# Kernel optimization log

Measured on AMD Instinct MI355X. Metric: run time of the kernel, lower is better.

Reference implementation:

```python
import jax, jax.numpy as jnp
import numpy as np

B, S, D = 4, 1024, 1024
H = 16
HD = D // H  # head_dim = 64


def setup_inputs() -> dict:
    key = jax.random.key(0)
    k1, k2, k3 = jax.random.split(key, 3)
    x = jax.random.normal(k1, (B, S, D), dtype=jnp.float32)
    # qkv_proj: Linear(input_dim, 3*embed_dim), stored as (in, out) for x @ W
    scale = 1.0 / np.sqrt(D)
    W_qkv = jax.random.uniform(k2, (D, 3 * D), dtype=jnp.float32, minval=-scale, maxval=scale)
    b_qkv = jax.random.uniform(k3, (3 * D,), dtype=jnp.float32, minval=-scale, maxval=scale)
    return {"x": x, "W_qkv": W_qkv, "b_qkv": b_qkv}


def reference(x, W_qkv, b_qkv):
    b, s, _ = x.shape
    qkv = x @ W_qkv + b_qkv                       # [B,S,3D]
    qkv = qkv.reshape(b, s, H, 3 * HD)            # [B,S,H,3*hd]
    qkv = qkv.transpose(0, 2, 1, 3)               # [B,H,S,3*hd]
    q, k, v = jnp.split(qkv, 3, axis=-1)          # each [B,H,S,hd]
    scores = jnp.einsum('bhqd,bhkd->bhqk', q, k) / jnp.sqrt(jnp.float32(HD))
    attn = jax.nn.softmax(scores, axis=-1)        # [B,H,S,S]
    out = jnp.einsum('bhqk,bhkd->bhqd', attn, v)  # [B,H,S,hd]
    values = out.transpose(0, 2, 1, 3).reshape(b, s, H * HD)  # [B,S,D]
    return values
```

## Files before the change

kernel.cpp:

```cpp
#include <hip/hip_runtime.h>
#include <hip/hip_bf16.h>
#include <stdint.h>

#define BATCH 4
#define SEQ 1024
#define DMODEL 1024
#define NH 16
#define HD 64

typedef __attribute__((ext_vector_type(8))) short short8;
typedef __attribute__((ext_vector_type(4))) float f32x4;
typedef __attribute__((ext_vector_type(4))) unsigned short ushort4v;

__device__ __forceinline__ unsigned short f2bf(float f) {
    union { float f; uint32_t u; } v; v.f = f;
    uint32_t r = v.u + 0x7fff + ((v.u >> 16) & 1);
    return (unsigned short)(r >> 16);
}

__device__ __forceinline__ uint32_t pack2bf(float lo, float hi) {
    union { __hip_bfloat162 h; uint32_t u; } cv;
    cv.h = __float22bfloat162_rn(make_float2(lo, hi));
    return cv.u;
}

__global__ __launch_bounds__(256) void prep_kernel(const float* __restrict__ x,
                                                   const float* __restrict__ W,
                                                   unsigned short* __restrict__ xb,
                                                   unsigned short* __restrict__ Wt) {
    __shared__ float tile[32][33];
    int bid = blockIdx.x;
    if (bid < 2048) {
        int t = bid * 256 + threadIdx.x;
        const float4* p = (const float4*)x + (size_t)t * 2;
        float4 a = p[0], b = p[1];
        short8 o;
        o[0] = (short)f2bf(a.x); o[1] = (short)f2bf(a.y);
        o[2] = (short)f2bf(a.z); o[3] = (short)f2bf(a.w);
        o[4] = (short)f2bf(b.x); o[5] = (short)f2bf(b.y);
        o[6] = (short)f2bf(b.z); o[7] = (short)f2bf(b.w);
        *((short8*)xb + t) = o;
    } else {
        int r = bid - 2048;
        int nb = (r % 96) * 32;
        int kb = (r / 96) * 32;
        int tx = threadIdx.x & 31;
        int ty = threadIdx.x >> 5;
#pragma unroll
        for (int i = 0; i < 4; i++) {
            int k = kb + ty + i * 8;
            tile[ty + i * 8][tx] = W[(size_t)k * 3072 + nb + tx];
        }
        __syncthreads();
#pragma unroll
        for (int i = 0; i < 4; i++) {
            int n = nb + ty + i * 8;
            Wt[(size_t)n * 1024 + kb + tx] = f2bf(tile[tx][ty + i * 8]);
        }
    }
}

#define BM 128
#define BN 128
#define BKK 64
#define QSCALE 0.18033688011112042f

__global__ __launch_bounds__(256, 3) void qkv_gemm_kernel(
    const unsigned short* __restrict__ xb,
    const unsigned short* __restrict__ wt,
    const float* __restrict__ bias,
    unsigned short* __restrict__ Qb,
    unsigned short* __restrict__ Kb,
    unsigned short* __restrict__ VbT)
{
    __shared__ __align__(16) unsigned short As[BM][64];
    __shared__ __align__(16) unsigned short Bs[BN][64];
    int tid = threadIdx.x;
    int wave = tid >> 6, lane = tid & 63;
    int quad = lane >> 4, l16 = lane & 15;
    int wm = wave >> 1, wn = wave & 1;

    int id = blockIdx.x;
    int x = id & 7, r = id >> 3;
    int m_t = (x & 3) * 8 + (r & 7);
    int n_t = (x >> 2) * 12 + (r >> 3);
    int m0 = m_t * BM;
    int n0 = n_t * BN;

    int grow = lane >> 3;
    int gcol = ((lane & 7) ^ grow) << 3;
    const unsigned short* gA = xb + (size_t)(m0 + wave * 32 + grow) * 1024 + gcol;
    const unsigned short* gB = wt + (size_t)(n0 + wave * 32 + grow) * 1024 + gcol;
    unsigned short* ldsA = &As[wave * 32][0] + lane * 8;
    unsigned short* ldsB = &Bs[wave * 32][0] + lane * 8;
    int sw = l16 & 7;

    short8 areg[4], breg[4];
#pragma unroll
    for (int i = 0; i < 4; i++) {
        areg[i] = *(const short8*)(gA + (size_t)i * 8 * 1024);
        breg[i] = *(const short8*)(gB + (size_t)i * 8 * 1024);
    }

    f32x4 acc[4][4] = {};
    for (int k0 = 0; k0 < 1024; k0 += BKK) {
        __syncthreads();
#pragma unroll
        for (int i = 0; i < 4; i++) {
            *(short8*)(ldsA + i * 512) = areg[i];
            *(short8*)(ldsB + i * 512) = breg[i];
        }
        __syncthreads();
        if (k0 + BKK < 1024) {
#pragma unroll
            for (int i = 0; i < 4; i++) {
                areg[i] = *(const short8*)(gA + (size_t)i * 8 * 1024 + k0 + BKK);
                breg[i] = *(const short8*)(gB + (size_t)i * 8 * 1024 + k0 + BKK);
            }
        }
#pragma unroll
        for (int kk = 0; kk < BKK; kk += 32) {
            int kb = kk >> 3;
            short8 af[4], bf[4];
#pragma unroll
            for (int t = 0; t < 4; t++) {
                int ar = wm * 64 + t * 16 + l16;
                af[t] = *(const short8*)&As[ar][((kb + quad) ^ sw) << 3];
            }
#pragma unroll
            for (int t = 0; t < 4; t++) {
                int br = wn * 64 + t * 16 + l16;
                bf[t] = *(const short8*)&Bs[br][((kb + quad) ^ sw) << 3];
            }
#pragma unroll
            for (int mt = 0; mt < 4; mt++)
#pragma unroll
                for (int nt = 0; nt < 4; nt++)
                    acc[mt][nt] = __builtin_amdgcn_mfma_f32_16x16x32_bf16(
                        af[mt], bf[nt], acc[mt][nt], 0, 0, 0);
        }
    }
#pragma unroll
    for (int nt = 0; nt < 4; nt++) {
        int n = n0 + wn * 64 + nt * 16 + l16;
        int h = n / 192;
        int c = n - h * 192;
        int which = c >> 6;
        int d = c & 63;
        float bv = bias[n];
        if (which == 2) {
#pragma unroll
            for (int mt = 0; mt < 4; mt++) {
                int m = m0 + wm * 64 + mt * 16 + quad * 4;
                int b = m >> 10, s = m & 1023;
                ushort4v o;
                o[0] = f2bf(acc[mt][nt][0] + bv);
                o[1] = f2bf(acc[mt][nt][1] + bv);
                o[2] = f2bf(acc[mt][nt][2] + bv);
                o[3] = f2bf(acc[mt][nt][3] + bv);
                *(ushort4v*)&VbT[((size_t)((b * 16 + h) * 64 + d)) * 1024 + s] = o;
            }
        } else {
            unsigned short* dst = (which == 0) ? Qb : Kb;
            float sc = (which == 0) ? QSCALE : 1.0f;
#pragma unroll
            for (int mt = 0; mt < 4; mt++) {
#pragma unroll
                for (int r2 = 0; r2 < 4; r2++) {
                    int m = m0 + wm * 64 + mt * 16 + quad * 4 + r2;
                    int b = m >> 10, s = m & 1023;
                    dst[((size_t)((b * 16 + h) * 1024 + s)) * 64 + d] = f2bf((acc[mt][nt][r2] + bv) * sc);
                }
            }
        }
    }
}

#define BQ 128
#define BKV 128

__global__ __launch_bounds__(256, 2) void attn_kernel(
    const unsigned short* __restrict__ Qb,
    const unsigned short* __restrict__ Kb,
    const unsigned short* __restrict__ VbT,
    float* __restrict__ out)
{
    __shared__ __align__(16) char smem[32768];
    __shared__ float lbuf[4][4][16];
    unsigned short (*Ks)[64]   = (unsigned short(*)[64])smem;
    unsigned short (*Vts)[128] = (unsigned short(*)[128])(smem + 16384);
    float* red = (float*)smem;

    int tid = threadIdx.x;
    int wave = tid >> 6, lane = tid & 63;
    int quad = lane >> 4, l16 = lane & 15;
    int qh = wave & 1, kh = wave >> 1;

    int id = blockIdx.x;
    int xcd = id & 7, rest = id >> 3;
    int qt = rest & 7, grp = rest >> 3;
    int bh = grp * 8 + xcd;
    int q0 = qt * BQ;

    const unsigned short* Qp = Qb + (size_t)bh * SEQ * HD;
    const unsigned short* Kp = Kb + (size_t)bh * SEQ * HD;
    const unsigned short* Vp = VbT + (size_t)bh * HD * SEQ;

    int f_k = (l16 & 3) | (((l16 >> 2) & 1) << 2);
    int f_v = l16 & 7;
    int prow = (kh << 6) + ((l16 >> 2) << 3) + (l16 & 3);

    short8 qf[4][2];
#pragma unroll
    for (int g = 0; g < 4; g++)
#pragma unroll
        for (int kc = 0; kc < 2; kc++)
            qf[g][kc] = *(const short8*)&Qp[(size_t)(q0 + qh * 64 + g * 16 + l16) * HD + kc * 32 + quad * 8];

    f32x4 oacc[4][4] = {};
    float lsum[4] = {0.f, 0.f, 0.f, 0.f};

    for (int kt = 0; kt < SEQ; kt += BKV) {
        __syncthreads();
#pragma unroll
        for (int i = 0; i < 4; i++) {
            int idx = i * 256 + tid;
            int krow = idx >> 3, kpb = idx & 7;
            int klb = kpb ^ ((krow & 3) | (((krow >> 3) & 1) << 2));
            *(short8*)&Ks[krow][kpb * 8] = *(const short8*)&Kp[(size_t)(kt + krow) * HD + klb * 8];
            int vrow = idx >> 4, vpb = idx & 15;
            int vlb = vpb ^ (vrow & 7);
            *(short8*)&Vts[vrow][vpb * 8] = *(const short8*)&Vp[(size_t)vrow * SEQ + kt + vlb * 8];
        }
        __syncthreads();

#pragma unroll
        for (int c = 0; c < 2; c++) {
            int base = prow + (c << 5);
            short8 kf0[2], kf1[2];
#pragma unroll
            for (int kc = 0; kc < 2; kc++) {
                kf0[kc] = *(const short8*)&Ks[base][(((kc << 2) + quad) ^ f_k) * 8];
                kf1[kc] = *(const short8*)&Ks[base + 4][(((kc << 2) + quad) ^ f_k) * 8];
            }
            short8 vf[4];
#pragma unroll
            for (int nt = 0; nt < 4; nt++)
                vf[nt] = *(const short8*)&Vts[nt * 16 + l16][(((kh << 3) + (c << 2) + quad) ^ f_v) * 8];
#pragma unroll
            for (int g = 0; g < 4; g++) {
                f32x4 s0 = {}, s1 = {};
#pragma unroll
                for (int kc = 0; kc < 2; kc++) {
                    s0 = __builtin_amdgcn_mfma_f32_16x16x32_bf16(kf0[kc], qf[g][kc], s0, 0, 0, 0);
                    s1 = __builtin_amdgcn_mfma_f32_16x16x32_bf16(kf1[kc], qf[g][kc], s1, 0, 0, 0);
                }
                float p0 = __builtin_amdgcn_exp2f(s0[0]);
                float p1 = __builtin_amdgcn_exp2f(s0[1]);
                float p2 = __builtin_amdgcn_exp2f(s0[2]);
                float p3 = __builtin_amdgcn_exp2f(s0[3]);
                float p4 = __builtin_amdgcn_exp2f(s1[0]);
                float p5 = __builtin_amdgcn_exp2f(s1[1]);
                float p6 = __builtin_amdgcn_exp2f(s1[2]);
                float p7 = __builtin_amdgcn_exp2f(s1[3]);
                lsum[g] += ((p0 + p1) + (p2 + p3)) + ((p4 + p5) + (p6 + p7));
                union { uint32_t w[4]; short8 s; } pf;
                pf.w[0] = pack2bf(p0, p1);
                pf.w[1] = pack2bf(p2, p3);
                pf.w[2] = pack2bf(p4, p5);
                pf.w[3] = pack2bf(p6, p7);
#pragma unroll
                for (int nt = 0; nt < 4; nt++)
                    oacc[g][nt] = __builtin_amdgcn_mfma_f32_16x16x32_bf16(vf[nt], pf.s, oacc[g][nt], 0, 0, 0);
            }
        }
    }

#pragma unroll
    for (int g = 0; g < 4; g++) {
        lsum[g] += __shfl_xor(lsum[g], 16, 64);
        lsum[g] += __shfl_xor(lsum[g], 32, 64);
    }
    int off = quad * 16 + l16;
    __syncthreads();
    if (kh == 1) {
        float* rp = red + qh * 4096;
#pragma unroll
        for (int g = 0; g < 4; g++)
#pragma unroll
            for (int nt = 0; nt < 4; nt++)
#pragma unroll
                for (int rr = 0; rr < 4; rr++)
                    rp[((g * 4 + nt) * 4 + rr) * 64 + off] = oacc[g][nt][rr];
        if (quad == 0)
#pragma unroll
            for (int g = 0; g < 4; g++) lbuf[wave][g][l16] = lsum[g];
    }
    __syncthreads();
    if (kh == 0) {
        float* rp = red + qh * 4096;
        int b = bh >> 4, h = bh & 15;
#pragma unroll
        for (int g = 0; g < 4; g++) {
            float l = lsum[g] + lbuf[wave + 2][g][l16];
            float inv = 1.f / l;
            int s = q0 + qh * 64 + g * 16 + l16;
#pragma unroll
            for (int nt = 0; nt < 4; nt++) {
                float4 o;
                o.x = (oacc[g][nt][0] + rp[((g * 4 + nt) * 4 + 0) * 64 + off]) * inv;
                o.y = (oacc[g][nt][1] + rp[((g * 4 + nt) * 4 + 1) * 64 + off]) * inv;
                o.z = (oacc[g][nt][2] + rp[((g * 4 + nt) * 4 + 2) * 64 + off]) * inv;
                o.w = (oacc[g][nt][3] + rp[((g * 4 + nt) * 4 + 3) * 64 + off]) * inv;
                *(float4*)&out[(size_t)(b * SEQ + s) * DMODEL + h * HD + nt * 16 + quad * 4] = o;
            }
        }
    }
}

extern "C" void kernel_launch(void* const* d_in, const int* in_sizes, int n_in,
                              void* d_out, int out_size, void* d_ws, size_t ws_size,
                              hipStream_t stream) {
    const float* x    = (const float*)d_in[0];
    const float* W    = (const float*)d_in[1];
    const float* bias = (const float*)d_in[2];
    float* out = (float*)d_out;
    char* ws = (char*)d_ws;

    unsigned short* xb  = (unsigned short*)(ws);
    unsigned short* wt  = (unsigned short*)(ws + 8388608);
    unsigned short* Qb  = (unsigned short*)(ws + 14680064);
    unsigned short* Kb  = (unsigned short*)(ws + 23068672);
    unsigned short* VbT = (unsigned short*)(ws + 31457280);

    prep_kernel<<<5120, 256, 0, stream>>>(x, W, xb, wt);
    qkv_gemm_kernel<<<768, 256, 0, stream>>>(xb, wt, bias, Qb, Kb, VbT);
    attn_kernel<<<512, 256, 0, stream>>>(Qb, Kb, VbT, out);
}
```

Measured before the change: 137.6 us.

## Fuse x bf16 conversion into QKV GEMM and double-buffer attention K/V tiles

The separate fp32-to-bf16 pass over x is removed. The QKV GEMM now loads fp32 x directly and packs it to bf16 before the LDS store, which eliminates a full write and reread of the converted activation. In exchange, every GEMM tile reads twice as many bytes for A, and that data is reread across the column tiles. Separately, the attention kernel gets two LDS buffers for K/V and prefetches the next tile into registers, dropping one barrier per iteration at the cost of 64KB of shared memory per block.

```diff
diff --git a/kernel.cpp b/kernel.cpp
--- a/kernel.cpp
+++ b/kernel.cpp
@@ -24,39 +24,24 @@
     return cv.u;
 }
 
-__global__ __launch_bounds__(256) void prep_kernel(const float* __restrict__ x,
-                                                   const float* __restrict__ W,
-                                                   unsigned short* __restrict__ xb,
+__global__ __launch_bounds__(256) void prep_kernel(const float* __restrict__ W,
                                                    unsigned short* __restrict__ Wt) {
     __shared__ float tile[32][33];
-    int bid = blockIdx.x;
-    if (bid < 2048) {
-        int t = bid * 256 + threadIdx.x;
-        const float4* p = (const float4*)x + (size_t)t * 2;
-        float4 a = p[0], b = p[1];
-        short8 o;
-        o[0] = (short)f2bf(a.x); o[1] = (short)f2bf(a.y);
-        o[2] = (short)f2bf(a.z); o[3] = (short)f2bf(a.w);
-        o[4] = (short)f2bf(b.x); o[5] = (short)f2bf(b.y);
-        o[6] = (short)f2bf(b.z); o[7] = (short)f2bf(b.w);
-        *((short8*)xb + t) = o;
-    } else {
-        int r = bid - 2048;
-        int nb = (r % 96) * 32;
-        int kb = (r / 96) * 32;
-        int tx = threadIdx.x & 31;
-        int ty = threadIdx.x >> 5;
-#pragma unroll
-        for (int i = 0; i < 4; i++) {
-            int k = kb + ty + i * 8;
-            tile[ty + i * 8][tx] = W[(size_t)k * 3072 + nb + tx];
-        }
-        __syncthreads();
-#pragma unroll
-        for (int i = 0; i < 4; i++) {
-            int n = nb + ty + i * 8;
-            Wt[(size_t)n * 1024 + kb + tx] = f2bf(tile[tx][ty + i * 8]);
-        }
+    int r = blockIdx.x;
+    int nb = (r % 96) * 32;
+    int kb = (r / 96) * 32;
+    int tx = threadIdx.x & 31;
+    int ty = threadIdx.x >> 5;
+#pragma unroll
+    for (int i = 0; i < 4; i++) {
+        int k = kb + ty + i * 8;
+        tile[ty + i * 8][tx] = W[(size_t)k * 3072 + nb + tx];
+    }
+    __syncthreads();
+#pragma unroll
+    for (int i = 0; i < 4; i++) {
+        int n = nb + ty + i * 8;
+        Wt[(size_t)n * 1024 + kb + tx] = f2bf(tile[tx][ty + i * 8]);
     }
 }
 
@@ -66,7 +51,7 @@
 #define QSCALE 0.18033688011112042f
 
 __global__ __launch_bounds__(256, 3) void qkv_gemm_kernel(
-    const unsigned short* __restrict__ xb,
+    const float* __restrict__ x,
     const unsigned short* __restrict__ wt,
     const float* __restrict__ bias,
     unsigned short* __restrict__ Qb,
@@ -81,24 +66,26 @@
     int wm = wave >> 1, wn = wave & 1;
 
     int id = blockIdx.x;
-    int x = id & 7, r = id >> 3;
-    int m_t = (x & 3) * 8 + (r & 7);
-    int n_t = (x >> 2) * 12 + (r >> 3);
+    int xc = id & 7, rr_ = id >> 3;
+    int m_t = (xc & 3) * 8 + (rr_ & 7);
+    int n_t = (xc >> 2) * 12 + (rr_ >> 3);
     int m0 = m_t * BM;
     int n0 = n_t * BN;
 
     int grow = lane >> 3;
     int gcol = ((lane & 7) ^ grow) << 3;
-    const unsigned short* gA = xb + (size_t)(m0 + wave * 32 + grow) * 1024 + gcol;
+    const float* gA = x + (size_t)(m0 + wave * 32 + grow) * 1024 + gcol;
     const unsigned short* gB = wt + (size_t)(n0 + wave * 32 + grow) * 1024 + gcol;
     unsigned short* ldsA = &As[wave * 32][0] + lane * 8;
     unsigned short* ldsB = &Bs[wave * 32][0] + lane * 8;
     int sw = l16 & 7;
 
-    short8 areg[4], breg[4];
+    float4 areg[4][2];
+    short8 breg[4];
 #pragma unroll
     for (int i = 0; i < 4; i++) {
-        areg[i] = *(const short8*)(gA + (size_t)i * 8 * 1024);
+        areg[i][0] = *(const float4*)(gA + (size_t)i * 8 * 1024);
+        areg[i][1] = *(const float4*)(gA + (size_t)i * 8 * 1024 + 4);
         breg[i] = *(const short8*)(gB + (size_t)i * 8 * 1024);
     }
 
@@ -107,14 +94,20 @@
         __syncthreads();
 #pragma unroll
         for (int i = 0; i < 4; i++) {
-            *(short8*)(ldsA + i * 512) = areg[i];
+            union { uint32_t w[4]; short8 s; } pk;
+            pk.w[0] = pack2bf(areg[i][0].x, areg[i][0].y);
+            pk.w[1] = pack2bf(areg[i][0].z, areg[i][0].w);
+            pk.w[2] = pack2bf(areg[i][1].x, areg[i][1].y);
+            pk.w[3] = pack2bf(areg[i][1].z, areg[i][1].w);
+            *(short8*)(ldsA + i * 512) = pk.s;
             *(short8*)(ldsB + i * 512) = breg[i];
         }
         __syncthreads();
         if (k0 + BKK < 1024) {
 #pragma unroll
             for (int i = 0; i < 4; i++) {
-                areg[i] = *(const short8*)(gA + (size_t)i * 8 * 1024 + k0 + BKK);
+                areg[i][0] = *(const float4*)(gA + (size_t)i * 8 * 1024 + k0 + BKK);
+                areg[i][1] = *(const float4*)(gA + (size_t)i * 8 * 1024 + k0 + BKK + 4);
                 breg[i] = *(const short8*)(gB + (size_t)i * 8 * 1024 + k0 + BKK);
             }
         }
@@ -185,10 +178,8 @@
     const unsigned short* __restrict__ VbT,
     float* __restrict__ out)
 {
-    __shared__ __align__(16) char smem[32768];
+    __shared__ __align__(16) char smem[65536];
     __shared__ float lbuf[4][4][16];
-    unsigned short (*Ks)[64]   = (unsigned short(*)[64])smem;
-    unsigned short (*Vts)[128] = (unsigned short(*)[128])(smem + 16384);
     float* red = (float*)smem;
 
     int tid = threadIdx.x;
@@ -217,21 +208,37 @@
         for (int kc = 0; kc < 2; kc++)
             qf[g][kc] = *(const short8*)&Qp[(size_t)(q0 + qh * 64 + g * 16 + l16) * HD + kc * 32 + quad * 8];
 
-    f32x4 oacc[4][4] = {};
-    float lsum[4] = {0.f, 0.f, 0.f, 0.f};
-
-    for (int kt = 0; kt < SEQ; kt += BKV) {
-        __syncthreads();
+    short8 kreg[4], vreg[4];
+    auto load_tile = [&](int kt) {
 #pragma unroll
         for (int i = 0; i < 4; i++) {
             int idx = i * 256 + tid;
             int krow = idx >> 3, kpb = idx & 7;
             int klb = kpb ^ ((krow & 3) | (((krow >> 3) & 1) << 2));
-            *(short8*)&Ks[krow][kpb * 8] = *(const short8*)&Kp[(size_t)(kt + krow) * HD + klb * 8];
+            kreg[i] = *(const short8*)&Kp[(size_t)(kt + krow) * HD + klb * 8];
             int vrow = idx >> 4, vpb = idx & 15;
             int vlb = vpb ^ (vrow & 7);
-            *(short8*)&Vts[vrow][vpb * 8] = *(const short8*)&Vp[(size_t)vrow * SEQ + kt + vlb * 8];
-        }
+            vreg[i] = *(const short8*)&Vp[(size_t)vrow * SEQ + kt + vlb * 8];
+        }
+    };
+    load_tile(0);
+
+    f32x4 oacc[4][4] = {};
+    float lsum[4] = {0.f, 0.f, 0.f, 0.f};
+
+    for (int t = 0; t < SEQ / BKV; t++) {
+        int p = t & 1;
+        unsigned short (*Ks)[64]   = (unsigned short(*)[64])(smem + p * 32768);
+        unsigned short (*Vts)[128] = (unsigned short(*)[128])(smem + p * 32768 + 16384);
+#pragma unroll
+        for (int i = 0; i < 4; i++) {
+            int idx = i * 256 + tid;
+            int krow = idx >> 3, kpb = idx & 7;
+            *(short8*)&Ks[krow][kpb * 8] = kreg[i];
+            int vrow = idx >> 4, vpb = idx & 15;
+            *(short8*)&Vts[vrow][vpb * 8] = vreg[i];
+        }
+        if (t + 1 < SEQ / BKV) load_tile((t + 1) * BKV);
         __syncthreads();
 
 #pragma unroll
@@ -327,13 +334,12 @@
     float* out = (float*)d_out;
     char* ws = (char*)d_ws;
 
-    unsigned short* xb  = (unsigned short*)(ws);
     unsigned short* wt  = (unsigned short*)(ws + 8388608);
     unsigned short* Qb  = (unsigned short*)(ws + 14680064);
     unsigned short* Kb  = (unsigned short*)(ws + 23068672);
     unsigned short* VbT = (unsigned short*)(ws + 31457280);
 
-    prep_kernel<<<5120, 256, 0, stream>>>(x, W, xb, wt);
-    qkv_gemm_kernel<<<768, 256, 0, stream>>>(xb, wt, bias, Qb, Kb, VbT);
+    prep_kernel<<<3072, 256, 0, stream>>>(W, wt);
+    qkv_gemm_kernel<<<768, 256, 0, stream>>>(x, wt, bias, Qb, Kb, VbT);
     attn_kernel<<<512, 256, 0, stream>>>(Qb, Kb, VbT, out);
 }
```

Measured after the change: 148.5 us. 7.9% more time.

## Load K/V fragments directly from global into registers, dropping LDS staging

Applied to the files above, without the earlier changes.

The attention kernel no longer stages K and V tiles through shared memory with block-wide barriers. Each wave now loads its K fragments straight from global memory into registers, double-buffering the next tile's fragments while computing the current one. V fragments are also loaded directly from global memory. This removes the LDS writes, reads and __syncthreads per KV tile, but every wave now fetches its fragments independently, which raises global/L2 traffic and register pressure. The unroll of the full KV loop may also enlarge the code.

```diff
diff --git a/kernel.cpp b/kernel.cpp
--- a/kernel.cpp
+++ b/kernel.cpp
@@ -81,9 +81,9 @@
     int wm = wave >> 1, wn = wave & 1;
 
     int id = blockIdx.x;
-    int x = id & 7, r = id >> 3;
-    int m_t = (x & 3) * 8 + (r & 7);
-    int n_t = (x >> 2) * 12 + (r >> 3);
+    int xc = id & 7, rr_ = id >> 3;
+    int m_t = (xc & 3) * 8 + (rr_ & 7);
+    int n_t = (xc >> 2) * 12 + (rr_ >> 3);
     int m0 = m_t * BM;
     int n0 = n_t * BN;
 
@@ -185,11 +185,8 @@
     const unsigned short* __restrict__ VbT,
     float* __restrict__ out)
 {
-    __shared__ __align__(16) char smem[32768];
+    __shared__ float red[8192];
     __shared__ float lbuf[4][4][16];
-    unsigned short (*Ks)[64]   = (unsigned short(*)[64])smem;
-    unsigned short (*Vts)[128] = (unsigned short(*)[128])(smem + 16384);
-    float* red = (float*)smem;
 
     int tid = threadIdx.x;
     int wave = tid >> 6, lane = tid & 63;
@@ -206,10 +203,6 @@
     const unsigned short* Kp = Kb + (size_t)bh * SEQ * HD;
     const unsigned short* Vp = VbT + (size_t)bh * HD * SEQ;
 
-    int f_k = (l16 & 3) | (((l16 >> 2) & 1) << 2);
-    int f_v = l16 & 7;
-    int prow = (kh << 6) + ((l16 >> 2) << 3) + (l16 & 3);
-
     short8 qf[4][2];
 #pragma unroll
     for (int g = 0; g < 4; g++)
@@ -217,43 +210,47 @@
         for (int kc = 0; kc < 2; kc++)
             qf[g][kc] = *(const short8*)&Qp[(size_t)(q0 + qh * 64 + g * 16 + l16) * HD + kc * 32 + quad * 8];
 
+    const unsigned short* kbase = Kp + (size_t)(kh * 64 + ((l16 >> 2) << 3) + (l16 & 3)) * HD + quad * 8;
+    const unsigned short* vbase = Vp + (size_t)l16 * SEQ + kh * 64 + quad * 8;
+
     f32x4 oacc[4][4] = {};
     float lsum[4] = {0.f, 0.f, 0.f, 0.f};
 
-    for (int kt = 0; kt < SEQ; kt += BKV) {
-        __syncthreads();
-#pragma unroll
-        for (int i = 0; i < 4; i++) {
-            int idx = i * 256 + tid;
-            int krow = idx >> 3, kpb = idx & 7;
-            int klb = kpb ^ ((krow & 3) | (((krow >> 3) & 1) << 2));
-            *(short8*)&Ks[krow][kpb * 8] = *(const short8*)&Kp[(size_t)(kt + krow) * HD + klb * 8];
-            int vrow = idx >> 4, vpb = idx & 15;
-            int vlb = vpb ^ (vrow & 7);
-            *(short8*)&Vts[vrow][vpb * 8] = *(const short8*)&Vp[(size_t)vrow * SEQ + kt + vlb * 8];
-        }
-        __syncthreads();
-
+    short8 kf[2][2][2][2];
+#pragma unroll
+    for (int c = 0; c < 2; c++)
+#pragma unroll
+        for (int t_ = 0; t_ < 2; t_++)
+#pragma unroll
+            for (int kc = 0; kc < 2; kc++)
+                kf[0][c][t_][kc] = *(const short8*)(kbase + (size_t)(c * 32 + t_ * 4) * HD + kc * 32);
+
+#pragma unroll
+    for (int t = 0; t < SEQ / BKV; t++) {
+        int kt = t * BKV;
+        int cur = t & 1, nxt = cur ^ 1;
+        if (t + 1 < SEQ / BKV) {
+#pragma unroll
+            for (int c = 0; c < 2; c++)
+#pragma unroll
+                for (int t_ = 0; t_ < 2; t_++)
+#pragma unroll
+                    for (int kc = 0; kc < 2; kc++)
+                        kf[nxt][c][t_][kc] = *(const short8*)(kbase + (size_t)(kt + BKV + c * 32 + t_ * 4) * HD + kc * 32);
+        }
 #pragma unroll
         for (int c = 0; c < 2; c++) {
-            int base = prow + (c << 5);
-            short8 kf0[2], kf1[2];
-#pragma unroll
-            for (int kc = 0; kc < 2; kc++) {
-                kf0[kc] = *(const short8*)&Ks[base][(((kc << 2) + quad) ^ f_k) * 8];
-                kf1[kc] = *(const short8*)&Ks[base + 4][(((kc << 2) + quad) ^ f_k) * 8];
-            }
             short8 vf[4];
 #pragma unroll
             for (int nt = 0; nt < 4; nt++)
-                vf[nt] = *(const short8*)&Vts[nt * 16 + l16][(((kh << 3) + (c << 2) + quad) ^ f_v) * 8];
+                vf[nt] = *(const short8*)(vbase + (size_t)nt * 16 * SEQ + kt + c * 32);
 #pragma unroll
             for (int g = 0; g < 4; g++) {
                 f32x4 s0 = {}, s1 = {};
 #pragma unroll
                 for (int kc = 0; kc < 2; kc++) {
-                    s0 = __builtin_amdgcn_mfma_f32_16x16x32_bf16(kf0[kc], qf[g][kc], s0, 0, 0, 0);
-                    s1 = __builtin_amdgcn_mfma_f32_16x16x32_bf16(kf1[kc], qf[g][kc], s1, 0, 0, 0);
+                    s0 = __builtin_amdgcn_mfma_f32_16x16x32_bf16(kf[cur][c][0][kc], qf[g][kc], s0, 0, 0, 0);
+                    s1 = __builtin_amdgcn_mfma_f32_16x16x32_bf16(kf[cur][c][1][kc], qf[g][kc], s1, 0, 0, 0);
                 }
                 float p0 = __builtin_amdgcn_exp2f(s0[0]);
                 float p1 = __builtin_amdgcn_exp2f(s0[1]);
@@ -282,7 +279,6 @@
         lsum[g] += __shfl_xor(lsum[g], 32, 64);
     }
     int off = quad * 16 + l16;
-    __syncthreads();
     if (kh == 1) {
         float* rp = red + qh * 4096;
 #pragma unroll
```

Result: slower. 144.6 us (+5.0%).
